# Optimization experiments

Hardware: AMD Instinct MI355X
Metric: run time of the kernel (lower is better)

## Reference

```python
import jax, jax.numpy as jnp
import numpy as np

D_MODEL = 768
NUM_HEADS = 12
HEAD_DIM = D_MODEL // NUM_HEADS
WINDOW_SIZE = 512
TOP_K = 64
SCALE = 1.0 / np.sqrt(HEAD_DIM).astype(np.float32)
NEG_INF = float('-inf')


def setup_inputs() -> dict:
    key = jax.random.key(0)
    ks = jax.random.split(key, 12)
    B, S, D = 2, 2048, D_MODEL
    std = 1.0 / np.sqrt(D)
    return {
        'query': jax.random.normal(ks[0], (B, S, D), jnp.float32),
        'key':   jax.random.normal(ks[1], (B, S, D), jnp.float32),
        'value': jax.random.normal(ks[2], (B, S, D), jnp.float32),
        'Wq': jax.random.normal(ks[3], (D, D), jnp.float32) * std,
        'bq': jnp.zeros((D,), jnp.float32),
        'Wk': jax.random.normal(ks[4], (D, D), jnp.float32) * std,
        'bk': jnp.zeros((D,), jnp.float32),
        'Wv': jax.random.normal(ks[5], (D, D), jnp.float32) * std,
        'bv': jnp.zeros((D,), jnp.float32),
        'Wo': jax.random.normal(ks[6], (D, D), jnp.float32) * std,
        'bo': jnp.zeros((D,), jnp.float32),
    }


def _split_heads(x, B, S):
    # [B,S,D] -> [B,H,S,hd]
    return x.reshape(B, S, NUM_HEADS, HEAD_DIM).transpose(0, 2, 1, 3)


def _forward(query, key, value, Wq, bq, Wk, bk, Wv, bv, Wo, bo):
    B, S, D = query.shape
    q = _split_heads(query @ Wq.T + bq, B, S)
    k = _split_heads(key @ Wk.T + bk, B, S)
    v = _split_heads(value @ Wv.T + bv, B, S)

    # dense scores [B,H,S,S]
    scores = jnp.einsum('bhqd,bhkd->bhqk', q, k) * SCALE

    # --- windowed (causal local) branch ---
    i = jnp.arange(S)[:, None]
    j = jnp.arange(S)[None, :]
    # window mask intersected with causal tril: i - ws//2 <= j <= i
    wmask = (j >= i - WINDOW_SIZE // 2) & (j <= i)  # [S,S]
    w_scores = jnp.where(wmask[None, None], scores, NEG_INF)
    w_probs = jax.nn.softmax(w_scores, axis=-1)
    ctx_w = jnp.einsum('bhqk,bhkd->bhqd', w_probs, v)

    # --- sparse top-k branch ---
    tk_vals, tk_idx = jax.lax.top_k(scores, TOP_K)  # [B,H,S,TOP_K]
    sparse = jnp.full_like(scores, NEG_INF)
    bi = jnp.arange(B)[:, None, None, None]
    hi = jnp.arange(NUM_HEADS)[None, :, None, None]
    si = jnp.arange(S)[None, None, :, None]
    sparse = sparse.at[bi, hi, si, tk_idx].set(tk_vals)
    s_probs = jax.nn.softmax(sparse, axis=-1)
    ctx_s = jnp.einsum('bhqk,bhkd->bhqd', s_probs, v)

    combined = (ctx_w + ctx_s) * 0.5  # [B,H,S,hd]
    combined = combined.transpose(0, 2, 1, 3).reshape(B, S, D)
    return combined @ Wo.T + bo


def reference(query, key, value, Wq, bq, Wk, bk, Wv, bv, Wo, bo):
    return _forward(query, key, value, Wq, bq, Wk, bk, Wv, bv, Wo, bo)
```

## Files before the change

### kernel.cpp

```cpp
#include <hip/hip_runtime.h>
#include <hip/hip_fp16.h>
#include <stdint.h>
#include <math.h>

#define NH    12
#define SEQ   2048
#define BATCH 2
#define DM    768
#define HD    64
#define SCALEF 0.125f

typedef unsigned short u16;
typedef unsigned int   u32;
typedef unsigned long long u64;
typedef __attribute__((ext_vector_type(8))) short bf16x8;
typedef __attribute__((ext_vector_type(8))) _Float16 h16x8;
typedef __attribute__((ext_vector_type(4))) float f32x4;

__device__ __forceinline__ u16 f2bf(float f){
  u32 u = __float_as_uint(f);
  u32 r = u + 0x7fffu + ((u >> 16) & 1u);
  return (u16)(r >> 16);
}
__device__ __forceinline__ float bf2f(u16 x){ return __uint_as_float(((u32)x) << 16); }
__device__ __forceinline__ u16 f2h(float f){ return __half_as_ushort(__float2half(f)); }
__device__ __forceinline__ float h2f(u16 x){ return __half2float(__ushort_as_half(x)); }

__device__ __forceinline__ float kval(u32 k){
  const u16 hb = (k & 0x8000u) ? (u16)(k & 0x7fffu) : (u16)(~k & 0xffffu);
  return h2f(hb);
}

__device__ __forceinline__ int dpp_sumi(int x){
  x += __builtin_amdgcn_update_dpp(0, x, 0x111, 0xf, 0xf, true);
  x += __builtin_amdgcn_update_dpp(0, x, 0x112, 0xf, 0xf, true);
  x += __builtin_amdgcn_update_dpp(0, x, 0x114, 0xf, 0xf, true);
  x += __builtin_amdgcn_update_dpp(0, x, 0x118, 0xf, 0xf, true);
  x += __builtin_amdgcn_update_dpp(0, x, 0x142, 0xa, 0xf, true);
  x += __builtin_amdgcn_update_dpp(0, x, 0x143, 0xc, 0xf, true);
  return __builtin_amdgcn_readlane(x, 63);
}
__device__ __forceinline__ int dpp_scan_incl(int x){
  x += __builtin_amdgcn_update_dpp(0, x, 0x111, 0xf, 0xf, true);
  x += __builtin_amdgcn_update_dpp(0, x, 0x112, 0xf, 0xf, true);
  x += __builtin_amdgcn_update_dpp(0, x, 0x114, 0xf, 0xf, true);
  x += __builtin_amdgcn_update_dpp(0, x, 0x118, 0xf, 0xf, true);
  x += __builtin_amdgcn_update_dpp(0, x, 0x142, 0xa, 0xf, true);
  x += __builtin_amdgcn_update_dpp(0, x, 0x143, 0xc, 0xf, true);
  return x;
}
__device__ __forceinline__ float dpp_sumf(float x){
  #define ASTEP(ctrl, rm) x += __int_as_float(__builtin_amdgcn_update_dpp(0, __float_as_int(x), ctrl, rm, 0xf, true));
  ASTEP(0x111,0xf) ASTEP(0x112,0xf) ASTEP(0x114,0xf) ASTEP(0x118,0xf) ASTEP(0x142,0xa) ASTEP(0x143,0xc)
  #undef ASTEP
  return __uint_as_float((u32)__builtin_amdgcn_readlane(__float_as_int(x), 63));
}
__device__ __forceinline__ float dpp_maxf(float x){
  #define MSTEP(ctrl, rm) { int o = __float_as_int(x); \
    x = fmaxf(x, __int_as_float(__builtin_amdgcn_update_dpp(o, o, ctrl, rm, 0xf, false))); }
  MSTEP(0x111,0xf) MSTEP(0x112,0xf) MSTEP(0x114,0xf) MSTEP(0x118,0xf) MSTEP(0x142,0xa) MSTEP(0x143,0xc)
  #undef MSTEP
  return __uint_as_float((u32)__builtin_amdgcn_readlane(__float_as_int(x), 63));
}
__device__ __forceinline__ int dpp_maxi(int x){
  #define ISTEP(ctrl, rm) { int o = x; int y = __builtin_amdgcn_update_dpp(o, o, ctrl, rm, 0xf, false); \
    x = (x > y) ? x : y; }
  ISTEP(0x111,0xf) ISTEP(0x112,0xf) ISTEP(0x114,0xf) ISTEP(0x118,0xf) ISTEP(0x142,0xa) ISTEP(0x143,0xc)
  #undef ISTEP
  return __builtin_amdgcn_readlane(x, 63);
}

__device__ __forceinline__ int pb_off(int q, int k){
  return (q << 11) + ((((k >> 3) ^ (q & 7)) << 3) | (k & 7));
}
__device__ __forceinline__ int ps_off(int kc, int q, int d){
  return (kc << 10) + (q << 6) + ((((d >> 2) ^ q) & 15) << 2) + (d & 3);
}

__global__ void cvt_kernel(const float* s0, const float* s1, const float* s2, const float* s3,
                           u16* d0, u16* d1, u16* d2, u16* d3, int n){
  const float* s; u16* d;
  switch (blockIdx.y){
    case 0: s = s0; d = d0; break;
    case 1: s = s1; d = d1; break;
    case 2: s = s2; d = d2; break;
    default: s = s3; d = d3; break;
  }
  int i = (blockIdx.x * 256 + threadIdx.x) * 4;
  if (i < n){
    float4 v = *(const float4*)(s + i);
    ushort4 o;
    o.x = f2bf(v.x); o.y = f2bf(v.y); o.z = f2bf(v.z); o.w = f2bf(v.w);
    *(ushort4*)(d + i) = o;
  }
}

template<int MODE>
__global__ __launch_bounds__(256) void gemm_bt(const u16* __restrict__ Aall, const u16* __restrict__ Wall,
      const float* __restrict__ bz0, const float* __restrict__ bz1, const float* __restrict__ bz2,
      u16* __restrict__ outb, float* __restrict__ outf){
  __shared__ u16 As[128][40];
  __shared__ u16 Bs[128][40];
  const int zz = blockIdx.z;
  const u16* A = Aall + (size_t)zz * 4096 * 768;
  const u16* W = Wall + (size_t)zz * 768 * 768;
  const float* bias = (zz == 0) ? bz0 : (zz == 1 ? bz1 : bz2);
  const int m0 = blockIdx.x * 128, n0 = blockIdx.y * 128;
  const int t = threadIdx.x, lane = t & 63, wv = t >> 6;
  const int wm = wv >> 1, wn = wv & 1;
  f32x4 acc[4][4] = {};
  const int arow = t >> 1, aseg = t & 1;
  const u16* ap = A + (size_t)(m0 + arow) * 768 + aseg * 16;
  const u16* bp = W + (size_t)(n0 + arow) * 768 + aseg * 16;
  for (int kt = 0; kt < 768; kt += 32){
    uint4 av0 = *(const uint4*)(ap + kt);
    uint4 av1 = *(const uint4*)(ap + kt + 8);
    uint4 bv0 = *(const uint4*)(bp + kt);
    uint4 bv1 = *(const uint4*)(bp + kt + 8);
    __syncthreads();
    *(uint4*)&As[arow][aseg*16]     = av0;
    *(uint4*)&As[arow][aseg*16 + 8] = av1;
    *(uint4*)&Bs[arow][aseg*16]     = bv0;
    *(uint4*)&Bs[arow][aseg*16 + 8] = bv1;
    __syncthreads();
    bf16x8 af[4], bq[4];
    #pragma unroll
    for (int i = 0; i < 4; ++i) af[i] = *(const bf16x8*)&As[wm*64 + i*16 + (lane & 15)][(lane >> 4) * 8];
    #pragma unroll
    for (int i = 0; i < 4; ++i) bq[i] = *(const bf16x8*)&Bs[wn*64 + i*16 + (lane & 15)][(lane >> 4) * 8];
    #pragma unroll
    for (int mi = 0; mi < 4; ++mi)
      #pragma unroll
      for (int ni = 0; ni < 4; ++ni)
        acc[mi][ni] = __builtin_amdgcn_mfma_f32_16x16x32_bf16(af[mi], bq[ni], acc[mi][ni], 0, 0, 0);
  }
  #pragma unroll
  for (int mi = 0; mi < 4; ++mi){
    #pragma unroll
    for (int ni = 0; ni < 4; ++ni){
      const int n = n0 + wn*64 + ni*16 + (lane & 15);
      const float bval = bias[n];
      const int mbase = m0 + wm*64 + mi*16 + (lane >> 4) * 4;
      if (MODE == 0 && zz == 2){
        const int bb = mbase >> 11, ss = mbase & 2047;
        const int hh = n >> 6, dd = n & 63;
        u64 pk = 0;
        #pragma unroll
        for (int r = 0; r < 4; ++r) pk |= (u64)f2h(acc[mi][ni][r] + bval) << (16 * r);
        *(u64*)(outb + (size_t)2 * 3145728 + (((size_t)(bb * NH + hh) * HD + dd) * SEQ + ss)) = pk;
      } else if (MODE == 0){
        #pragma unroll
        for (int r = 0; r < 4; ++r){
          const int m = mbase + r;
          const int bb = m >> 11, ss = m & 2047, hh = n >> 6, dd = n & 63;
          outb[(size_t)zz * 3145728 + (((size_t)bb * NH + hh) * SEQ + ss) * HD + dd] = f2bf(acc[mi][ni][r] + bval);
        }
      } else {
        #pragma unroll
        for (int r = 0; r < 4; ++r){
          const int m = mbase + r;
          outf[(size_t)m * DM + n] = acc[mi][ni][r] + bval;
        }
      }
    }
  }
}

__global__ __launch_bounds__(1024, 8) void attn7_kernel(const u16* __restrict__ Qh,
      const u16* __restrict__ Kh, const u16* __restrict__ Vt, u16* __restrict__ ctxb){
  __shared__ __align__(16) u32 smem[20480];
  u16*  Pm    = (u16*)smem;
  float* psum = (float*)(smem + 16384);

  const int q0 = blockIdx.x * 16;
  const int h = blockIdx.y, b = blockIdx.z, bh = b * NH + h;
  const int t = threadIdx.x, lane = t & 63, w = t >> 6;
  const u16* Qb  = Qh + ((size_t)bh * SEQ + q0) * HD;
  const u16* Kb  = Kh + (size_t)bh * SEQ * HD;
  const u16* Vtb = Vt + (size_t)bh * HD * SEQ;

  {
    const int qcol = lane & 15;
    const bf16x8 qa0 = *(const bf16x8*)(Qb + qcol * HD + (lane >> 4) * 8);
    const bf16x8 qa1 = *(const bf16x8*)(Qb + qcol * HD + 32 + (lane >> 4) * 8);
    #pragma unroll 4
    for (int tile = 0; tile < 8; ++tile){
      const int kr = w * 128 + tile * 16 + (lane & 15);
      const bf16x8 ka0 = *(const bf16x8*)(Kb + (size_t)kr * HD + (lane >> 4) * 8);
      const bf16x8 ka1 = *(const bf16x8*)(Kb + (size_t)kr * HD + 32 + (lane >> 4) * 8);
      f32x4 d = {};
      d = __builtin_amdgcn_mfma_f32_16x16x32_bf16(ka0, qa0, d, 0, 0, 0);
      d = __builtin_amdgcn_mfma_f32_16x16x32_bf16(ka1, qa1, d, 0, 0, 0);
      const int kbase = w * 128 + tile * 16 + (lane >> 4) * 4;
      const u32 lo = (u32)f2h(d[0] * SCALEF) | ((u32)f2h(d[1] * SCALEF) << 16);
      const u32 hi = (u32)f2h(d[2] * SCALEF) | ((u32)f2h(d[3] * SCALEF) << 16);
      const int off = (qcol << 10) | ((kbase >> 1) ^ (qcol << 1));
      *(u64*)(smem + off) = (u64)lo | ((u64)hi << 32);
    }
  }
  __syncthreads();

  const int qi = q0 + w;
  const int sw = w << 1;
  u32* rowp = smem + (w << 10);
  u32* cand = smem + 16384 + (w << 8);
  u32 ukp[16];
  #pragma unroll
  for (int i = 0; i < 16; ++i){
    const u32 dw = rowp[(lane + 64 * i) ^ sw];
    const u32 s = (dw >> 15) & 0x00010001u;
    ukp[i] = dw ^ (0x80008000u | (s * 0x7fffu));
  }
  __asm__ volatile("" ::: "memory");

  u32 pmx = ukp[0];
  #pragma unroll
  for (int i = 1; i < 16; ++i){
    const u32 a = ukp[i];
    const u32 l = (a & 0xffffu) > (pmx & 0xffffu) ? (a & 0xffffu) : (pmx & 0xffffu);
    const u32 hh = (a >> 16) > (pmx >> 16) ? (a >> 16) : (pmx >> 16);
    pmx = l | (hh << 16);
  }
  u32 Mk = (pmx & 0xffffu) > (pmx >> 16) ? (pmx & 0xffffu) : (pmx >> 16);
  Mk = (u32)dpp_maxi((int)Mk);
  const float m1 = kval(Mk);

  u32 blo = 0;  int c_lo = 2048;
  u32 bhi = Mk + 1; int c_hi = 0;
  {
    u32 tm = (Mk > 1024u) ? (Mk - 1024u) : 1u;
    if (tm >= bhi) tm = (blo + bhi) >> 1;
    #pragma unroll 1
    for (int it = 0; it < 12; ++it){
      int cl = 0;
      #pragma unroll
      for (int i = 0; i < 16; ++i){
        cl += ((ukp[i] & 0xffffu) >= tm) ? 1 : 0;
        cl += ((ukp[i] >> 16) >= tm) ? 1 : 0;
      }
      const int c = dpp_sumi(cl);
      if (c >= 64){ blo = tm; c_lo = c; if (c <= 240) break; }
      else        { bhi = tm; c_hi = c; }
      const u32 nt = (blo + bhi) >> 1;
      if (nt == blo) break;
      tm = nt;
    }
  }

  int n_c;
  {
    int cl = 0;
    #pragma unroll
    for (int i = 0; i < 16; ++i){
      cl += ((ukp[i] & 0xffffu) >= blo) ? 1 : 0;
      cl += ((ukp[i] >> 16) >= blo) ? 1 : 0;
    }
    const int incl = dpp_scan_incl(cl);
    const int totalc = __builtin_amdgcn_readlane(incl, 63);
    int pos = incl - cl;
    #pragma unroll
    for (int i = 0; i < 16; ++i){
      #pragma unroll
      for (int hh = 0; hh < 2; ++hh){
        const u32 kk = hh ? (ukp[i] >> 16) : (ukp[i] & 0xffffu);
        if (kk >= blo && pos < 256){
          const int idx = 2 * lane + (i << 7) + hh;
          cand[pos] = (kk << 16) | (u32)(2047 - idx);
          ++pos;
        }
      }
    }
    n_c = totalc < 256 ? totalc : 256;
  }
  __asm__ volatile("s_waitcnt lgkmcnt(0)" ::: "memory");

  u32 cj[4];
  #pragma unroll
  for (int j = 0; j < 4; ++j){
    const int s = lane + 64 * j;
    const u32 vv = cand[s];
    cj[j] = (s < n_c) ? vv : 0u;
  }
  while (bhi - blo > 1u){
    const u32 tm = (blo + bhi) >> 1;
    const u32 kthr = tm << 16;
    int cl = 0;
    #pragma unroll
    for (int j = 0; j < 4; ++j) cl += (cj[j] >= kthr) ? 1 : 0;
    const int c = dpp_sumi(cl);
    if (c >= 64){ blo = tm; c_lo = c; } else { bhi = tm; c_hi = c; }
  }
  const u32 T = blo;
  const int G = c_hi;
  const int r_need = 64 - G;

  float ev[4]; int eqc = 0;
  float zl = 0.f;
  #pragma unroll
  for (int j = 0; j < 4; ++j){
    const u32 key = cj[j] >> 16;
    ev[j] = __expf(kval(key) - m1);
    zl += (key > T) ? ev[j] : 0.f;
    eqc += (key == T) ? 1 : 0;
  }
  const int pre_eq = dpp_scan_incl(eqc) - eqc;
  const float eT = __expf(kval(T) - m1);
  const float Z1 = dpp_sumf(zl) + (float)r_need * eT;
  const float inv1 = 0.5f / Z1;

  const int start = (qi - 256 > 0) ? (qi - 256) : 0;
  float wvv[5];
  #pragma unroll
  for (int it = 0; it < 5; ++it){
    const int c0 = start + lane + it * 64;
    const int c = (c0 <= qi) ? c0 : qi;
    const u32 dw = rowp[(c >> 1) ^ sw];
    const u16 hb = (c & 1) ? (u16)(dw >> 16) : (u16)(dw & 0xffffu);
    wvv[it] = (c0 <= qi) ? h2f(hb) : -INFINITY;
  }
  float wm = -INFINITY;
  #pragma unroll
  for (int it = 0; it < 5; ++it) wm = fmaxf(wm, wvv[it]);
  wm = dpp_maxf(wm);
  float zs = 0.f;
  #pragma unroll
  for (int it = 0; it < 5; ++it){
    const int c = start + lane + it * 64;
    if (c <= qi){ const float e = __expf(wvv[it] - wm); wvv[it] = e; zs += e; }
  }
  zs = dpp_sumf(zs);
  const float inv = 0.5f / zs;

  {
    uint4* prow = (uint4*)(Pm + (w << 11));
    const uint4 z4 = {0u, 0u, 0u, 0u};
    #pragma unroll
    for (int i = 0; i < 4; ++i) prow[lane + i * 64] = z4;
    __asm__ volatile("" ::: "memory");
    #pragma unroll
    for (int it = 0; it < 5; ++it){
      const int c = start + lane + it * 64;
      if (c <= qi) Pm[pb_off(w, c)] = f2h(wvv[it] * inv);
    }
    __asm__ volatile("" ::: "memory");
    int rloc = pre_eq;
    #pragma unroll
    for (int j = 0; j < 4; ++j){
      const u32 key = cj[j] >> 16;
      const bool isgt = key > T;
      const bool iseq = (key == T);
      const bool sel = isgt || (iseq && rloc < r_need);
      if (iseq) ++rloc;
      if (sel){
        const int idx = 2047 - (int)(cj[j] & 0x7ffu);
        u16* cell = &Pm[pb_off(w, idx)];
        *cell = f2h(h2f(*cell) + ev[j] * inv1);
      }
    }
  }
  __syncthreads();

  {
    const int kc = w >> 2, mi = w & 3;
    f32x4 acc = {};
    #pragma unroll 4
    for (int ks = 0; ks < 16; ++ks){
      const int kk = kc * 512 + ks * 32;
      const h16x8 va = *(const h16x8*)(Vtb + (size_t)(mi * 16 + (lane & 15)) * SEQ + kk + (lane >> 4) * 8);
      const h16x8 pf = *(const h16x8*)&Pm[pb_off(lane & 15, kk + (lane >> 4) * 8)];
      acc = __builtin_amdgcn_mfma_f32_16x16x32_f16(va, pf, acc, 0, 0, 0);
    }
    const int q = lane & 15, dbase = mi * 16 + (lane >> 4) * 4;
    *(f32x4*)&psum[ps_off(kc, q, dbase)] = acc;
  }
  __syncthreads();

  {
    const int q = t >> 6, d = t & 63;
    const float r = psum[ps_off(0, q, d)] + psum[ps_off(1, q, d)]
                  + psum[ps_off(2, q, d)] + psum[ps_off(3, q, d)];
    ctxb[((size_t)(b * SEQ + q0 + q)) * DM + h * HD + d] = f2bf(r);
  }
}

extern "C" void kernel_launch(void* const* d_in, const int* in_sizes, int n_in,
                              void* d_out, int out_size, void* d_ws, size_t ws_size,
                              hipStream_t stream){
  const float* q_in = (const float*)d_in[0];
  const float* k_in = (const float*)d_in[1];
  const float* v_in = (const float*)d_in[2];
  const float* Wq = (const float*)d_in[3];
  const float* bq = (const float*)d_in[4];
  const float* Wk = (const float*)d_in[5];
  const float* bk = (const float*)d_in[6];
  const float* Wv = (const float*)d_in[7];
  const float* bv = (const float*)d_in[8];
  const float* Wo = (const float*)d_in[9];
  const float* bo = (const float*)d_in[10];

  char* ws = (char*)d_ws;
  u16* Xb   = (u16*)ws;
  u16* Wb   = (u16*)(ws + 18874368);
  u16* QKVh = (u16*)(ws + 23592960);
  u16* ctxb = (u16*)(ws + 42467328);

  cvt_kernel<<<dim3(3145728 / 1024, 3), 256, 0, stream>>>(
      q_in, k_in, v_in, nullptr, Xb, Xb + 3145728, Xb + 2 * 3145728, nullptr, 3145728);
  cvt_kernel<<<dim3(589824 / 1024, 4), 256, 0, stream>>>(
      Wq, Wk, Wv, Wo, Wb, Wb + 589824, Wb + 2 * 589824, Wb + 3 * 589824, 589824);

  gemm_bt<0><<<dim3(32, 6, 3), 256, 0, stream>>>(Xb, Wb, bq, bk, bv, QKVh, nullptr);

  attn7_kernel<<<dim3(SEQ / 16, NH, BATCH), 1024, 0, stream>>>(
      QKVh, QKVh + 3145728, QKVh + 2 * 3145728, ctxb);

  gemm_bt<1><<<dim3(32, 6, 1), 256, 0, stream>>>(
      ctxb, Wb + 3 * 589824, bo, bo, bo, nullptr, (float*)d_out);
}
```

Measured before the change: 305.5 us.

## Store sortable keys in LDS and rescan rows instead of holding them in registers

Each score is converted to its order-preserving unsigned key once, when the QK^T tile is written to shared memory, instead of after every load. The 16-register per-lane key array is removed. Each bisection pass now rereads the row from LDS as 128-bit vector loads, with the XOR swizzle changed to match the wider access, and the row max is found with a packed rotate-and-compare. This is meant to lower register pressure for the 1024-thread blocks, at the cost of extra LDS traffic on every threshold-counting iteration.

```diff
diff --git a/kernel.cpp b/kernel.cpp
--- a/kernel.cpp
+++ b/kernel.cpp
@@ -22,13 +22,16 @@
   u32 r = u + 0x7fffu + ((u >> 16) & 1u);
   return (u16)(r >> 16);
 }
-__device__ __forceinline__ float bf2f(u16 x){ return __uint_as_float(((u32)x) << 16); }
 __device__ __forceinline__ u16 f2h(float f){ return __half_as_ushort(__float2half(f)); }
 __device__ __forceinline__ float h2f(u16 x){ return __half2float(__ushort_as_half(x)); }
 
 __device__ __forceinline__ float kval(u32 k){
   const u16 hb = (k & 0x8000u) ? (u16)(k & 0x7fffu) : (u16)(~k & 0xffffu);
   return h2f(hb);
+}
+__device__ __forceinline__ u32 rot16(u32 x){ return __builtin_amdgcn_alignbit(x, x, 16); }
+__device__ __forceinline__ int cnt_ge(u32 dw, u32 tm){
+  return (int)((dw & 0xffffu) >= tm) + (int)((dw >> 16) >= tm);
 }
 
 __device__ __forceinline__ int dpp_sumi(int x){
@@ -166,7 +169,7 @@
   }
 }
 
-__global__ __launch_bounds__(1024, 8) void attn7_kernel(const u16* __restrict__ Qh,
+__global__ __launch_bounds__(1024, 8) void attn9_kernel(const u16* __restrict__ Qh,
       const u16* __restrict__ Kh, const u16* __restrict__ Vt, u16* __restrict__ ctxb){
   __shared__ __align__(16) u32 smem[20480];
   u16*  Pm    = (u16*)smem;
@@ -192,54 +195,56 @@
       d = __builtin_amdgcn_mfma_f32_16x16x32_bf16(ka0, qa0, d, 0, 0, 0);
       d = __builtin_amdgcn_mfma_f32_16x16x32_bf16(ka1, qa1, d, 0, 0, 0);
       const int kbase = w * 128 + tile * 16 + (lane >> 4) * 4;
-      const u32 lo = (u32)f2h(d[0] * SCALEF) | ((u32)f2h(d[1] * SCALEF) << 16);
-      const u32 hi = (u32)f2h(d[2] * SCALEF) | ((u32)f2h(d[3] * SCALEF) << 16);
-      const int off = (qcol << 10) | ((kbase >> 1) ^ (qcol << 1));
+      u32 lo = (u32)f2h(d[0] * SCALEF) | ((u32)f2h(d[1] * SCALEF) << 16);
+      u32 hi = (u32)f2h(d[2] * SCALEF) | ((u32)f2h(d[3] * SCALEF) << 16);
+      const u32 s0 = (lo >> 15) & 0x00010001u;
+      const u32 s1 = (hi >> 15) & 0x00010001u;
+      lo ^= 0x80008000u | (s0 * 0x7fffu);
+      hi ^= 0x80008000u | (s1 * 0x7fffu);
+      const int off = (qcol << 10) | ((kbase >> 1) ^ (qcol << 2));
       *(u64*)(smem + off) = (u64)lo | ((u64)hi << 32);
     }
   }
   __syncthreads();
 
   const int qi = q0 + w;
-  const int sw = w << 1;
-  u32* rowp = smem + (w << 10);
-  u32* cand = smem + 16384 + (w << 8);
-  u32 ukp[16];
-  #pragma unroll
-  for (int i = 0; i < 16; ++i){
-    const u32 dw = rowp[(lane + 64 * i) ^ sw];
-    const u32 s = (dw >> 15) & 0x00010001u;
-    ukp[i] = dw ^ (0x80008000u | (s * 0x7fffu));
-  }
-  __asm__ volatile("" ::: "memory");
-
-  u32 pmx = ukp[0];
-  #pragma unroll
-  for (int i = 1; i < 16; ++i){
-    const u32 a = ukp[i];
-    const u32 l = (a & 0xffffu) > (pmx & 0xffffu) ? (a & 0xffffu) : (pmx & 0xffffu);
-    const u32 hh = (a >> 16) > (pmx >> 16) ? (a >> 16) : (pmx >> 16);
-    pmx = l | (hh << 16);
-  }
-  u32 Mk = (pmx & 0xffffu) > (pmx >> 16) ? (pmx & 0xffffu) : (pmx >> 16);
-  Mk = (u32)dpp_maxi((int)Mk);
+  uint4* row4 = (uint4*)smem + (w << 8);
+  u32*  rowp  = smem + (w << 10);
+  u32*  cand  = smem + 16384 + (w << 8);
+  const int x4 = w;
+
+  u32 mx = 0;
+  #pragma unroll
+  for (int ii = 0; ii < 4; ++ii){
+    const uint4 v = row4[(lane + 64 * ii) ^ x4];
+    const u32 m0 = v.x > rot16(v.x) ? v.x : rot16(v.x);
+    const u32 m1_ = v.y > rot16(v.y) ? v.y : rot16(v.y);
+    const u32 m2 = v.z > rot16(v.z) ? v.z : rot16(v.z);
+    const u32 m3 = v.w > rot16(v.w) ? v.w : rot16(v.w);
+    u32 mm = m0 > m1_ ? m0 : m1_;
+    mm = mm > m2 ? mm : m2;
+    mm = mm > m3 ? mm : m3;
+    mx = mx > mm ? mx : mm;
+  }
+  const u32 Mk = (u32)dpp_maxi((int)(mx >> 16));
   const float m1 = kval(Mk);
 
-  u32 blo = 0;  int c_lo = 2048;
+  u32 blo = 0;
   u32 bhi = Mk + 1; int c_hi = 0;
   {
     u32 tm = (Mk > 1024u) ? (Mk - 1024u) : 1u;
     if (tm >= bhi) tm = (blo + bhi) >> 1;
     #pragma unroll 1
     for (int it = 0; it < 12; ++it){
+      __asm__ volatile("" ::: "memory");
       int cl = 0;
       #pragma unroll
-      for (int i = 0; i < 16; ++i){
-        cl += ((ukp[i] & 0xffffu) >= tm) ? 1 : 0;
-        cl += ((ukp[i] >> 16) >= tm) ? 1 : 0;
+      for (int ii = 0; ii < 4; ++ii){
+        const uint4 v = row4[(lane + 64 * ii) ^ x4];
+        cl += cnt_ge(v.x, tm) + cnt_ge(v.y, tm) + cnt_ge(v.z, tm) + cnt_ge(v.w, tm);
       }
       const int c = dpp_sumi(cl);
-      if (c >= 64){ blo = tm; c_lo = c; if (c <= 240) break; }
+      if (c >= 64){ blo = tm; if (c <= 240) break; }
       else        { bhi = tm; c_hi = c; }
       const u32 nt = (blo + bhi) >> 1;
       if (nt == blo) break;
@@ -249,24 +254,31 @@
 
   int n_c;
   {
+    __asm__ volatile("" ::: "memory");
     int cl = 0;
     #pragma unroll
-    for (int i = 0; i < 16; ++i){
-      cl += ((ukp[i] & 0xffffu) >= blo) ? 1 : 0;
-      cl += ((ukp[i] >> 16) >= blo) ? 1 : 0;
+    for (int ii = 0; ii < 4; ++ii){
+      const uint4 v = row4[(lane + 64 * ii) ^ x4];
+      cl += cnt_ge(v.x, blo) + cnt_ge(v.y, blo) + cnt_ge(v.z, blo) + cnt_ge(v.w, blo);
     }
     const int incl = dpp_scan_incl(cl);
     const int totalc = __builtin_amdgcn_readlane(incl, 63);
     int pos = incl - cl;
-    #pragma unroll
-    for (int i = 0; i < 16; ++i){
+    __asm__ volatile("" ::: "memory");
+    #pragma unroll
+    for (int ii = 0; ii < 4; ++ii){
+      const uint4 v = row4[(lane + 64 * ii) ^ x4];
+      const u32 dws[4] = {v.x, v.y, v.z, v.w};
       #pragma unroll
-      for (int hh = 0; hh < 2; ++hh){
-        const u32 kk = hh ? (ukp[i] >> 16) : (ukp[i] & 0xffffu);
-        if (kk >= blo && pos < 256){
-          const int idx = 2 * lane + (i << 7) + hh;
-          cand[pos] = (kk << 16) | (u32)(2047 - idx);
-          ++pos;
+      for (int c4 = 0; c4 < 4; ++c4){
+        #pragma unroll
+        for (int hh = 0; hh < 2; ++hh){
+          const u32 kk = hh ? (dws[c4] >> 16) : (dws[c4] & 0xffffu);
+          if (kk >= blo && pos < 256){
+            const int idx = 8 * (lane + 64 * ii) + 2 * c4 + hh;
+            cand[pos] = (kk << 16) | (u32)(2047 - idx);
+            ++pos;
+          }
         }
       }
     }
@@ -288,7 +300,7 @@
     #pragma unroll
     for (int j = 0; j < 4; ++j) cl += (cj[j] >= kthr) ? 1 : 0;
     const int c = dpp_sumi(cl);
-    if (c >= 64){ blo = tm; c_lo = c; } else { bhi = tm; c_hi = c; }
+    if (c >= 64){ blo = tm; } else { bhi = tm; c_hi = c; }
   }
   const u32 T = blo;
   const int G = c_hi;
@@ -314,9 +326,9 @@
   for (int it = 0; it < 5; ++it){
     const int c0 = start + lane + it * 64;
     const int c = (c0 <= qi) ? c0 : qi;
-    const u32 dw = rowp[(c >> 1) ^ sw];
-    const u16 hb = (c & 1) ? (u16)(dw >> 16) : (u16)(dw & 0xffffu);
-    wvv[it] = (c0 <= qi) ? h2f(hb) : -INFINITY;
+    const u32 dw = rowp[(c >> 1) ^ (w << 2)];
+    const u32 kk = (c & 1) ? (dw >> 16) : (dw & 0xffffu);
+    wvv[it] = (c0 <= qi) ? kval(kk) : -INFINITY;
   }
   float wm = -INFINITY;
   #pragma unroll
@@ -411,7 +423,7 @@
 
   gemm_bt<0><<<dim3(32, 6, 3), 256, 0, stream>>>(Xb, Wb, bq, bk, bv, QKVh, nullptr);
 
-  attn7_kernel<<<dim3(SEQ / 16, NH, BATCH), 1024, 0, stream>>>(
+  attn9_kernel<<<dim3(SEQ / 16, NH, BATCH), 1024, 0, stream>>>(
       QKVh, QKVh + 3145728, QKVh + 2 * 3145728, ctxb);
 
   gemm_bt<1><<<dim3(32, 6, 1), 256, 0, stream>>>(
```

New measurement: 298.2 us. -2.4%, faster.
